# Kernel tuning notes

Hardware: AMD Instinct MI355X
Metric: run time of the kernel (lower is better)

The kernel has to match this reference:

```python
import jax, jax.numpy as jnp
import numpy as np

B, S, D, R = 8, 512, 1024, 128

def setup_inputs() -> dict:
    key = jax.random.key(0)
    k1, k2 = jax.random.split(key)
    batch = jax.random.normal(k1, (B, S, D), dtype=jnp.float32)
    # nn.init.uniform_(proj, -0.05, 0.05)
    proj = jax.random.uniform(k2, (D, R), dtype=jnp.float32, minval=-0.05, maxval=0.05)
    return {"batch": batch, "proj": proj}

def reference(batch, proj):
    # transformed: [B, S, R]
    transformed = jnp.matmul(batch, proj)
    # pairwise squared distances via broadcast diff (same math as expand/transpose/diff/pow/sum)
    diffs = transformed[:, :, None, :] - transformed[:, None, :, :]  # [B, S, S, R]
    squared_distances = jnp.sum(diffs * diffs, axis=-1)              # [B, S, S]
    return squared_distances
```

## Files before the change

kernel.cpp:

```cpp
#include <hip/hip_runtime.h>
#include <hip/hip_bf16.h>

constexpr int B_ = 8;
constexpr int S_ = 512;
constexpr int D_ = 1024;
constexpr int R_ = 128;
constexpr int M_ = B_ * S_;

typedef unsigned short u16;
typedef __attribute__((ext_vector_type(8))) short short8;
typedef __attribute__((ext_vector_type(4))) float f32x4;

static __device__ __forceinline__ u16 f2bf(float f) {
    unsigned u = __float_as_uint(f);
    u += 0x7fffu + ((u >> 16) & 1u);
    return (u16)(u >> 16);
}
static __device__ __forceinline__ float bf2f(u16 u) {
    return __uint_as_float((unsigned)u << 16);
}

__global__ __launch_bounds__(256) void transpose_proj_kernel(
    const float* __restrict__ P, u16* __restrict__ Pt)
{
    __shared__ float S[16][132];
    const int t  = threadIdx.x;
    const int kk = blockIdx.x;
    const int kq = blockIdx.y;

#pragma unroll
    for (int p = 0; p < 2; ++p) {
        const int k = (t >> 5) + p * 8;
        const int c = (t & 31) * 4;
        *reinterpret_cast<float4*>(&S[k][c]) =
            *reinterpret_cast<const float4*>(
                &P[(size_t)(kk * 64 + kq * 16 + k) * R_ + c]);
    }
    __syncthreads();

    const int col = t >> 1;
    const int h   = t & 1;
    unsigned u[4];
#pragma unroll
    for (int q = 0; q < 4; ++q) {
        const u16 lo = f2bf(S[h * 8 + q * 2 + 0][col]);
        const u16 hi = f2bf(S[h * 8 + q * 2 + 1][col]);
        u[q] = (unsigned)lo | ((unsigned)hi << 16);
    }
    *reinterpret_cast<uint4*>(&Pt[(size_t)kk * 8192 + col * 64 + kq * 16 + h * 8]) =
        make_uint4(u[0], u[1], u[2], u[3]);
}

__global__ __launch_bounds__(256) void gemm1_kernel(
    const float* __restrict__ A,
    const u16* __restrict__ Pt,
    u16* __restrict__ T)
{
    __shared__ u16 As[16][72];
    __shared__ u16 Bs[64][72];

    const int t    = threadIdx.x;
    const int row0 = blockIdx.y * 16;
    const int col0 = blockIdx.x * 64;
    const int w    = t >> 6;
    const int l    = t & 63;
    const int g    = l >> 4;
    const int l15  = l & 15;

    f32x4 acc = f32x4{0.f, 0.f, 0.f, 0.f};

    const int ar = t >> 4;
    const int aq = t & 15;
    const int bcol = t >> 2;
    const int bq   = t & 3;

    const float* Arow = &A[(size_t)(row0 + ar) * D_];

    float4 a_pf = *reinterpret_cast<const float4*>(&Arow[aq * 4]);
    const uint4* bsrc = reinterpret_cast<const uint4*>(
        &Pt[(size_t)0 * 8192 + (col0 + bcol) * 64 + bq * 16]);
    uint4 b_pf0 = bsrc[0];
    uint4 b_pf1 = bsrc[1];

    for (int kk = 0; kk < 16; ++kk) {
        {
            const u16 c0 = f2bf(a_pf.x), c1 = f2bf(a_pf.y),
                      c2 = f2bf(a_pf.z), c3 = f2bf(a_pf.w);
            const unsigned lo = (unsigned)c0 | ((unsigned)c1 << 16);
            const unsigned hi = (unsigned)c2 | ((unsigned)c3 << 16);
            *reinterpret_cast<uint2*>(&As[ar][aq * 4]) = make_uint2(lo, hi);
            uint4* bdst = reinterpret_cast<uint4*>(&Bs[bcol][bq * 16]);
            bdst[0] = b_pf0;
            bdst[1] = b_pf1;
        }
        if (kk + 1 < 16) {
            a_pf = *reinterpret_cast<const float4*>(&Arow[(kk + 1) * 64 + aq * 4]);
            const uint4* bs = reinterpret_cast<const uint4*>(
                &Pt[(size_t)(kk + 1) * 8192 + (col0 + bcol) * 64 + bq * 16]);
            b_pf0 = bs[0];
            b_pf1 = bs[1];
        }
        __syncthreads();

#pragma unroll
        for (int h2 = 0; h2 < 2; ++h2) {
            const short8 a = *reinterpret_cast<const short8*>(
                &As[l15][h2 * 32 + g * 8]);
            const short8 b = *reinterpret_cast<const short8*>(
                &Bs[w * 16 + l15][h2 * 32 + g * 8]);
            acc = __builtin_amdgcn_mfma_f32_16x16x32_bf16(a, b, acc, 0, 0, 0);
        }
        __syncthreads();
    }

#pragma unroll
    for (int r = 0; r < 4; ++r) {
        const int row = row0 + g * 4 + r;
        const int col = col0 + w * 16 + l15;
        T[(size_t)row * R_ + col] = f2bf(acc[r]);
    }
}

__global__ __launch_bounds__(256) void pairdist_kernel(
    const u16* __restrict__ T,
    float* __restrict__ out)
{
    __shared__ u16 Ti[64][136];
    __shared__ u16 Tj[64][136];
    __shared__ float ni[64], nj[64];

    const int t  = threadIdx.x;
    const int b  = blockIdx.z;
    const int i0 = blockIdx.y * 64;
    const int j0 = blockIdx.x * 64;
    const u16* Tb = T + (size_t)b * S_ * R_;

    const int w   = t >> 6;
    const int l   = t & 63;
    const int g   = l >> 4;
    const int l15 = l & 15;

    {
        const int r  = t >> 2;
        const int kq = (t & 3) * 32;
        const uint4* si = reinterpret_cast<const uint4*>(&Tb[(size_t)(i0 + r) * R_ + kq]);
        const uint4* sj = reinterpret_cast<const uint4*>(&Tb[(size_t)(j0 + r) * R_ + kq]);
        uint4* di = reinterpret_cast<uint4*>(&Ti[r][kq]);
        uint4* dj = reinterpret_cast<uint4*>(&Tj[r][kq]);
#pragma unroll
        for (int p = 0; p < 4; ++p) { di[p] = si[p]; dj[p] = sj[p]; }
    }
    __syncthreads();

    if (t < 128) {
        const u16* rowp = (t < 64) ? &Ti[t][0] : &Tj[t - 64][0];
        float s = 0.f;
#pragma unroll
        for (int p = 0; p < 16; ++p) {
            const uint4 v = *reinterpret_cast<const uint4*>(rowp + p * 8);
            const unsigned uu[4] = {v.x, v.y, v.z, v.w};
#pragma unroll
            for (int q = 0; q < 4; ++q) {
                const float f0 = bf2f((u16)(uu[q] & 0xffffu));
                const float f1 = bf2f((u16)(uu[q] >> 16));
                s += f0 * f0 + f1 * f1;
            }
        }
        if (t < 64) ni[t] = s; else nj[t - 64] = s;
    }
    __syncthreads();

    f32x4 acc[4];
#pragma unroll
    for (int n = 0; n < 4; ++n) acc[n] = f32x4{0.f, 0.f, 0.f, 0.f};

#pragma unroll
    for (int kk = 0; kk < 4; ++kk) {
        const short8 a = *reinterpret_cast<const short8*>(
            &Ti[w * 16 + l15][kk * 32 + g * 8]);
#pragma unroll
        for (int n = 0; n < 4; ++n) {
            const short8 bb = *reinterpret_cast<const short8*>(
                &Tj[n * 16 + l15][kk * 32 + g * 8]);
            acc[n] = __builtin_amdgcn_mfma_f32_16x16x32_bf16(a, bb, acc[n], 0, 0, 0);
        }
    }

    float niv[4];
#pragma unroll
    for (int r = 0; r < 4; ++r) niv[r] = ni[w * 16 + g * 4 + r];
#pragma unroll
    for (int n = 0; n < 4; ++n) {
        const float njv = nj[n * 16 + l15];
#pragma unroll
        for (int r = 0; r < 4; ++r) {
            const int row = i0 + w * 16 + g * 4 + r;
            const int col = j0 + n * 16 + l15;
            out[((size_t)b * S_ + row) * S_ + col] = niv[r] + njv - 2.f * acc[n][r];
        }
    }
}

extern "C" void kernel_launch(void* const* d_in, const int* in_sizes, int n_in,
                              void* d_out, int out_size, void* d_ws, size_t ws_size,
                              hipStream_t stream) {
    const float* batch = (const float*)d_in[0];
    const float* proj  = (const float*)d_in[1];
    float* out = (float*)d_out;

    u16* Pt = (u16*)d_ws;
    u16* T  = Pt + 16 * 8192;

    transpose_proj_kernel<<<dim3(16, 4), 256, 0, stream>>>(proj, Pt);
    gemm1_kernel<<<dim3(2, M_ / 16), 256, 0, stream>>>(batch, Pt, T);
    pairdist_kernel<<<dim3(S_ / 64, S_ / 64, B_), 256, 0, stream>>>(T, out);
}
```

Baseline: 77.22 us.

## Compute full projection width per block, preload A rows, double-buffer LDS

The GEMM1 kernel now has each block cover all 128 output columns instead of splitting them across two blocks, so each activation row is read and converted once rather than twice. All 16 A chunks are prefetched into registers up front. LDS is double-buffered so one barrier per k-step replaces two. The costs are higher register pressure from 16 float4 registers, fewer blocks (256), and more LDS per block.

```diff
diff --git a/kernel.cpp b/kernel.cpp
--- a/kernel.cpp
+++ b/kernel.cpp
@@ -56,68 +56,85 @@
     const u16* __restrict__ Pt,
     u16* __restrict__ T)
 {
-    __shared__ u16 As[16][72];
-    __shared__ u16 Bs[64][72];
+    __shared__ u16 As[2][16][72];
+    __shared__ u16 Bs[2][128][72];
 
     const int t    = threadIdx.x;
-    const int row0 = blockIdx.y * 16;
-    const int col0 = blockIdx.x * 64;
+    const int row0 = blockIdx.x * 16;
     const int w    = t >> 6;
     const int l    = t & 63;
     const int g    = l >> 4;
     const int l15  = l & 15;
 
-    f32x4 acc = f32x4{0.f, 0.f, 0.f, 0.f};
+    f32x4 acc[2];
+    acc[0] = f32x4{0.f, 0.f, 0.f, 0.f};
+    acc[1] = f32x4{0.f, 0.f, 0.f, 0.f};
 
     const int ar = t >> 4;
     const int aq = t & 15;
-    const int bcol = t >> 2;
-    const int bq   = t & 3;
-
-    const float* Arow = &A[(size_t)(row0 + ar) * D_];
-
-    float4 a_pf = *reinterpret_cast<const float4*>(&Arow[aq * 4]);
-    const uint4* bsrc = reinterpret_cast<const uint4*>(
-        &Pt[(size_t)0 * 8192 + (col0 + bcol) * 64 + bq * 16]);
-    uint4 b_pf0 = bsrc[0];
-    uint4 b_pf1 = bsrc[1];
-
+    const int bcol = t >> 1;
+    const int bh   = t & 1;
+
+    const float* Abase = &A[(size_t)(row0 + ar) * D_ + aq * 4];
+
+    float4 areg[16];
+#pragma unroll
+    for (int kk = 0; kk < 16; ++kk)
+        areg[kk] = *reinterpret_cast<const float4*>(Abase + kk * 64);
+
+    const uint4* b0src = reinterpret_cast<const uint4*>(
+        &Pt[(size_t)0 * 8192 + bcol * 64 + bh * 32]);
+    uint4 bp0 = b0src[0];
+    uint4 bp1 = b0src[1];
+    uint4 bp2 = b0src[2];
+    uint4 bp3 = b0src[3];
+
+#pragma unroll
     for (int kk = 0; kk < 16; ++kk) {
+        const int cur = kk & 1;
         {
-            const u16 c0 = f2bf(a_pf.x), c1 = f2bf(a_pf.y),
-                      c2 = f2bf(a_pf.z), c3 = f2bf(a_pf.w);
+            const float4 v = areg[kk];
+            const u16 c0 = f2bf(v.x), c1 = f2bf(v.y), c2 = f2bf(v.z), c3 = f2bf(v.w);
             const unsigned lo = (unsigned)c0 | ((unsigned)c1 << 16);
             const unsigned hi = (unsigned)c2 | ((unsigned)c3 << 16);
-            *reinterpret_cast<uint2*>(&As[ar][aq * 4]) = make_uint2(lo, hi);
-            uint4* bdst = reinterpret_cast<uint4*>(&Bs[bcol][bq * 16]);
-            bdst[0] = b_pf0;
-            bdst[1] = b_pf1;
+            *reinterpret_cast<uint2*>(&As[cur][ar][aq * 4]) = make_uint2(lo, hi);
+            uint4* bdst = reinterpret_cast<uint4*>(&Bs[cur][bcol][bh * 32]);
+            bdst[0] = bp0;
+            bdst[1] = bp1;
+            bdst[2] = bp2;
+            bdst[3] = bp3;
         }
         if (kk + 1 < 16) {
-            a_pf = *reinterpret_cast<const float4*>(&Arow[(kk + 1) * 64 + aq * 4]);
             const uint4* bs = reinterpret_cast<const uint4*>(
-                &Pt[(size_t)(kk + 1) * 8192 + (col0 + bcol) * 64 + bq * 16]);
-            b_pf0 = bs[0];
-            b_pf1 = bs[1];
+                &Pt[(size_t)(kk + 1) * 8192 + bcol * 64 + bh * 32]);
+            bp0 = bs[0];
+            bp1 = bs[1];
+            bp2 = bs[2];
+            bp3 = bs[3];
         }
         __syncthreads();
 
 #pragma unroll
         for (int h2 = 0; h2 < 2; ++h2) {
             const short8 a = *reinterpret_cast<const short8*>(
-                &As[l15][h2 * 32 + g * 8]);
-            const short8 b = *reinterpret_cast<const short8*>(
-                &Bs[w * 16 + l15][h2 * 32 + g * 8]);
-            acc = __builtin_amdgcn_mfma_f32_16x16x32_bf16(a, b, acc, 0, 0, 0);
-        }
-        __syncthreads();
-    }
-
-#pragma unroll
-    for (int r = 0; r < 4; ++r) {
-        const int row = row0 + g * 4 + r;
-        const int col = col0 + w * 16 + l15;
-        T[(size_t)row * R_ + col] = f2bf(acc[r]);
+                &As[cur][l15][h2 * 32 + g * 8]);
+#pragma unroll
+            for (int n = 0; n < 2; ++n) {
+                const short8 b = *reinterpret_cast<const short8*>(
+                    &Bs[cur][w * 32 + n * 16 + l15][h2 * 32 + g * 8]);
+                acc[n] = __builtin_amdgcn_mfma_f32_16x16x32_bf16(a, b, acc[n], 0, 0, 0);
+            }
+        }
+    }
+
+#pragma unroll
+    for (int n = 0; n < 2; ++n) {
+#pragma unroll
+        for (int r = 0; r < 4; ++r) {
+            const int row = row0 + g * 4 + r;
+            const int col = w * 32 + n * 16 + l15;
+            T[(size_t)row * R_ + col] = f2bf(acc[n][r]);
+        }
     }
 }
 
@@ -212,6 +229,6 @@
     u16* T  = Pt + 16 * 8192;
 
     transpose_proj_kernel<<<dim3(16, 4), 256, 0, stream>>>(proj, Pt);
-    gemm1_kernel<<<dim3(2, M_ / 16), 256, 0, stream>>>(batch, Pt, T);
+    gemm1_kernel<<<M_ / 16, 256, 0, stream>>>(batch, Pt, T);
     pairdist_kernel<<<dim3(S_ / 64, S_ / 64, B_), 256, 0, stream>>>(T, out);
 }
```

After: 80.29 us. 4.0% more time.
